# Kernel tuning notes

Hardware: AMD Instinct MI355X
Metric: run time of the kernel (lower is better)

Reference implementation:

```python
import jax, jax.numpy as jnp
import numpy as np

N = 50000; E = 200000; H = 128; L = 3; T = 2; FOUT = 64
G = 1000; NP = 3; ATOM_V = 64; BOND_V = 8
EPS = 1e-5
_DEG_HIST = np.array([0., 50000., 75000., 50000., 25000.])
# PyG PNAConv: avg_deg['log'] = sum(hist[d] * log(d+1)) / num_nodes
AVG_DEG_LOG = float((np.log(np.arange(5) + 1.0) * _DEG_HIST).sum() / _DEG_HIST.sum())


def _bn(v, g, b):
    # training-mode BatchNorm1d (biased variance), eps=1e-5
    mu = v.mean(0)
    var = ((v - mu) ** 2).mean(0)
    return (v - mu) * jax.lax.rsqrt(var + EPS) * g + b


def setup_inputs() -> dict:
    key = jax.random.key(0)
    ks = jax.random.split(key, 16)
    def nrm(k, shape, fan):
        return (jax.random.normal(k, shape, dtype=jnp.float32) / np.sqrt(fan)).astype(jnp.float32)
    return {
        'x': jax.random.randint(ks[0], (N, 9), 0, ATOM_V),
        'edge_index': jax.random.randint(ks[1], (2, E), 0, N),
        'batch': jnp.sort(jax.random.randint(ks[2], (N,), 0, G)),
        'edge_attr_idx': jax.random.randint(ks[3], (E, 3), 0, BOND_V),
        'atom_emb': nrm(ks[4], (9, ATOM_V, H), H),
        'bond_emb': nrm(ks[5], (3, BOND_V, H), H),
        'edge_W': nrm(ks[6], (L, H, H), H), 'edge_b': jnp.zeros((L, H), jnp.float32),
        'pre_W': nrm(ks[7], (L, T, 3 * H, H), 3 * H), 'pre_b': jnp.zeros((L, T, H), jnp.float32),
        'post_W': nrm(ks[8], (L, T, 13 * H, FOUT), 13 * H), 'post_b': jnp.zeros((L, T, FOUT), jnp.float32),
        'lin_W': nrm(ks[9], (L, H, H), H), 'lin_b': jnp.zeros((L, H), jnp.float32),
        'bn_g': jnp.ones((L, H), jnp.float32), 'bn_b': jnp.zeros((L, H), jnp.float32),
        'mlp_W': nrm(ks[10], (2, H, H), H), 'mlp_b': jnp.zeros((2, H), jnp.float32),
        'mlp_g': jnp.ones((2, H), jnp.float32), 'mlp_be': jnp.zeros((2, H), jnp.float32),
        'hW1': nrm(ks[11], (H, H // 2), H), 'hb1': jnp.zeros((H // 2,), jnp.float32),
        'hg1': jnp.ones((H // 2,), jnp.float32), 'hbe1': jnp.zeros((H // 2,), jnp.float32),
        'hW2': nrm(ks[12], (H // 2, H // 4), H // 2), 'hb2': jnp.zeros((H // 4,), jnp.float32),
        'hg2': jnp.ones((H // 4,), jnp.float32), 'hbe2': jnp.zeros((H // 4,), jnp.float32),
        'hW3': nrm(ks[13], (H // 4, NP), H // 4), 'hb3': jnp.zeros((NP,), jnp.float32),
    }


def reference(x, edge_index, batch, edge_attr_idx, atom_emb, bond_emb,
              edge_W, edge_b, pre_W, pre_b, post_W, post_b, lin_W, lin_b,
              bn_g, bn_b, mlp_W, mlp_b, mlp_g, mlp_be,
              hW1, hb1, hg1, hbe1, hW2, hb2, hg2, hbe2, hW3, hb3):
    # encoders: sum of per-feature embeddings (OGB Atom/Bond encoder)
    h = atom_emb[jnp.arange(9), x].sum(1)               # [N,H]
    e = bond_emb[jnp.arange(3), edge_attr_idx].sum(1)   # [E,H]
    src, dst = edge_index[0], edge_index[1]
    cnt = jax.ops.segment_sum(jnp.ones((E,), jnp.float32), dst, N)
    deg = jnp.maximum(cnt, 1.0)[:, None, None]          # clamp(1), as in PyG scalers
    amp = jnp.log(deg + 1.0) / AVG_DEG_LOG
    att = AVG_DEG_LOG / jnp.log(deg + 1.0)
    has = (cnt > 0)[:, None, None]
    for l in range(L):
        ea = e @ edge_W[l] + edge_b[l]                                  # [E,H]
        msg_in = jnp.concatenate([h[dst], h[src], ea], -1)              # [E,3H]
        m = jnp.einsum('ef,tfh->eth', msg_in, pre_W[l]) + pre_b[l]      # [E,T,H]
        s1 = jax.ops.segment_sum(m, dst, N)
        s2 = jax.ops.segment_sum(m * m, dst, N)
        mean = s1 / deg
        std = jnp.sqrt(jax.nn.relu(s2 / deg - mean * mean) + EPS)
        mn = jnp.where(has, jax.ops.segment_min(m, dst, N), 0.0)
        mx = jnp.where(has, jax.ops.segment_max(m, dst, N), 0.0)
        agg = jnp.concatenate([mean, mn, mx, std], -1)                  # [N,T,4H]
        scaled = jnp.concatenate([agg, agg * amp, agg * att], -1)       # [N,T,12H]
        upd = jnp.concatenate(
            [jnp.broadcast_to(h[:, None, :], (N, T, H)), scaled], -1)   # [N,T,13H]
        o = jnp.einsum('ntf,tfo->nto', upd, post_W[l]) + post_b[l]      # [N,T,FOUT]
        o = o.reshape(N, T * FOUT) @ lin_W[l] + lin_b[l]                # [N,H]
        h = jax.nn.relu(_bn(o, bn_g[l], bn_b[l]))
    g = jax.ops.segment_sum(h, batch, G)                                # [G,H]
    for i in range(2):
        g = jax.nn.relu(_bn(g @ mlp_W[i] + mlp_b[i], mlp_g[i], mlp_be[i]))
    g = jax.nn.relu(_bn(g @ hW1 + hb1, hg1, hbe1))
    g = jax.nn.relu(_bn(g @ hW2 + hb2, hg2, hbe2))
    return g @ hW3 + hb3                                                # [G,NP]
```

## Files before the change

### kernel.cpp

```cpp
#include <hip/hip_runtime.h>
#include <math.h>


#define NN 50000
#define NE 200000
#define HD 128
#define NG 1000
#define EPSV 1e-5f
#define ALOGC 1.1330197327247628f

#define AP 1288
#define OPF 132
#define SCB 49

typedef __bf16 bf16x8 __attribute__((ext_vector_type(8)));
typedef float f32x4 __attribute__((ext_vector_type(4)));

__device__ __forceinline__ unsigned short f2bf(float f) {
    unsigned int u = __float_as_uint(f);
    unsigned int r = (u + 0x7FFFu + ((u >> 16) & 1u)) >> 16;
    return (unsigned short)r;
}
__device__ __forceinline__ float bf2f(unsigned short h) {
    return __uint_as_float((unsigned int)h << 16);
}

__global__ void k_fill(float* __restrict__ o, float v, int n) {
    int i = blockIdx.x * 256 + threadIdx.x;
    if (i < n) o[i] = v;
}

__global__ void k_zero(float* __restrict__ z, int n) {
    int i = blockIdx.x * 256 + threadIdx.x;
    if (i < n) z[i] = 0.f;
}

__global__ __launch_bounds__(256) void k_encode_nodes(
    const int* __restrict__ x, const float* __restrict__ aemb, float* __restrict__ h) {
    __shared__ int xi[8][9];
    int nb = blockIdx.x * 8;
    int tid = threadIdx.x;
    if (tid < 72) xi[tid / 9][tid % 9] = x[nb * 9 + tid];
    __syncthreads();
    int node = tid >> 5, c4 = (tid & 31) * 4;
    float4 acc = make_float4(0.f, 0.f, 0.f, 0.f);
#pragma unroll
    for (int f = 0; f < 9; ++f) {
        float4 e = *(const float4*)(aemb + (size_t)(f * 64 + xi[node][f]) * HD + c4);
        acc.x += e.x; acc.y += e.y; acc.z += e.z; acc.w += e.w;
    }
    *(float4*)(h + (size_t)(nb + node) * HD + c4) = acc;
}

__global__ void k_count(const int* __restrict__ dst, int* __restrict__ cnt) {
    int e = blockIdx.x * 256 + threadIdx.x;
    if (e < NE) atomicAdd(&cnt[dst[e]], 1);
}

__global__ __launch_bounds__(1024) void k_scanA(const int* __restrict__ cnt,
                                                int* __restrict__ sc, int* __restrict__ tot) {
    __shared__ int buf[1024];
    int tid = threadIdx.x;
    int i = blockIdx.x * 1024 + tid;
    int v = (i < NN) ? cnt[i] : 0;
    buf[tid] = v;
    __syncthreads();
    for (int s = 1; s < 1024; s <<= 1) {
        int t = (tid >= s) ? buf[tid - s] : 0;
        __syncthreads();
        buf[tid] += t;
        __syncthreads();
    }
    if (i < NN) sc[i] = buf[tid];
    if (tid == 1023) tot[blockIdx.x] = buf[1023];
}

__global__ void k_scanB(const int* __restrict__ tot, int* __restrict__ offb) {
    if (threadIdx.x == 0) {
        int run = 0;
        for (int b = 0; b < SCB; ++b) { offb[b] = run; run += tot[b]; }
    }
}

__global__ __launch_bounds__(1024) void k_scanC(
    const int* __restrict__ cnt, const int* __restrict__ sc, const int* __restrict__ offb,
    int* __restrict__ rowptr, float* __restrict__ ampv, float* __restrict__ attv) {
    int i = blockIdx.x * 1024 + threadIdx.x;
    if (i == 0) rowptr[0] = 0;
    if (i < NN) {
        rowptr[i + 1] = offb[blockIdx.x] + sc[i];
        int v = cnt[i];
        float dg = (float)(v > 0 ? v : 1);
        float lg = logf(dg + 1.0f);
        ampv[i] = lg / ALOGC;
        attv[i] = ALOGC / lg;
    }
}

__global__ void k_scatter(const int* __restrict__ ei, const int* __restrict__ eai,
                          const int* __restrict__ rowptr,
                          int* __restrict__ fill, int* __restrict__ precs) {
    int e = blockIdx.x * 256 + threadIdx.x;
    if (e < NE) {
        int d = ei[NE + e];
        int pos = rowptr[d] + atomicAdd(&fill[d], 1);
        int cidx = eai[e * 3] | (eai[e * 3 + 1] << 3) | (eai[e * 3 + 2] << 6);
        precs[pos] = ei[e] | (cidx << 17);
    }
}

__global__ void k_fold(const float* __restrict__ edge_W, const float* __restrict__ edge_b,
                       const float* __restrict__ pre_W, const float* __restrict__ pre_b,
                       float* __restrict__ cW, float* __restrict__ tb) {
    int l = blockIdx.y;
    int k = blockIdx.x;
    int tj = threadIdx.x;
    int t = tj >> 7, j = tj & 127;
    const float* pw = pre_W + ((size_t)(l * 2 + t) * 384 + 256) * 128 + j;
    if (k < 128) {
        const float* ew = edge_W + ((size_t)l * 128 + k) * 128;
        float acc = 0.f;
        for (int i = 0; i < 128; ++i) acc += ew[i] * pw[i * 128];
        cW[((size_t)l * 128 + k) * 256 + tj] = acc;
    } else {
        const float* eb = edge_b + l * 128;
        float acc = pre_b[(l * 2 + t) * 128 + j];
        for (int i = 0; i < 128; ++i) acc += eb[i] * pw[i * 128];
        tb[l * 256 + tj] = acc;
    }
}

__global__ void k_bcomb2(const float* __restrict__ bemb, const float* __restrict__ cW,
                         unsigned short* __restrict__ bcomb) {
    int ci = blockIdx.x, l = blockIdx.y, tj = threadIdx.x;
    const float* s0 = bemb + (size_t)(0 * 8 + (ci & 7)) * 128;
    const float* s1 = bemb + (size_t)(1 * 8 + ((ci >> 3) & 7)) * 128;
    const float* s2 = bemb + (size_t)(2 * 8 + (ci >> 6)) * 128;
    const float* w = cW + (size_t)l * 128 * 256;
    float acc = 0.f;
    for (int i = 0; i < 128; ++i) acc += (s0[i] + s1[i] + s2[i]) * w[i * 256 + tj];
    bcomb[((size_t)l * 512 + ci) * 256 + tj] = f2bf(acc);
}

__device__ __forceinline__ void pack_body2(const float* __restrict__ W, int N, int NT,
                                           unsigned short* __restrict__ pkh,
                                           unsigned short* __restrict__ pkl,
                                           int blk, int lane) {
    int kstep = blk / NT, nt = blk - kstep * NT;
    int kb = kstep * 32 + (lane >> 4) * 8;
    int col = nt * 16 + (lane & 15);
    unsigned short th[8], tl[8];
#pragma unroll
    for (int i = 0; i < 8; ++i) {
        float w = W[(size_t)(kb + i) * N + col];
        unsigned short hh = f2bf(w);
        th[i] = hh;
        tl[i] = f2bf(w - bf2f(hh));
    }
    size_t base = ((size_t)blk * 64 + lane) * 8;
    *(uint4*)(pkh + base) = *(uint4*)th;
    *(uint4*)(pkl + base) = *(uint4*)tl;
}

__global__ __launch_bounds__(64) void k_packall(
    const float* __restrict__ post_W, const float* __restrict__ lin_W,
    const float* __restrict__ pre_W,
    unsigned short* __restrict__ pkPostHi, unsigned short* __restrict__ pkPostLo,
    unsigned short* __restrict__ pkLinHi, unsigned short* __restrict__ pkLinLo,
    unsigned short* __restrict__ pkPreHi, unsigned short* __restrict__ pkPreLo) {
    int b = blockIdx.x;
    int lane = threadIdx.x;
    if (b < 1248) {
        int l = b / 416, rem = b % 416;
        int t = rem / 208, blk = rem % 208;
        size_t off = ((size_t)l * 2 + t) * 106496;
        pack_body2(post_W + ((size_t)l * 2 + t) * 1664 * 64, 64, 4,
                   pkPostHi + off, pkPostLo + off, blk, lane);
    } else if (b < 1344) {
        int idx = b - 1248;
        int l = idx / 32, blk = idx % 32;
        pack_body2(lin_W + (size_t)l * 128 * 128, 128, 8,
                   pkLinHi + (size_t)l * 16384, pkLinLo + (size_t)l * 16384, blk, lane);
    } else {
        int idx = b - 1344;
        int l = idx / 128, bb = idx % 128;
        const float* preW = pre_W + (size_t)l * 2 * 384 * 128;
        unsigned short* phi = pkPreHi + (size_t)l * 65536;
        unsigned short* plo = pkPreLo + (size_t)l * 65536;
        int kstep = bb >> 5, nt = bb & 31;
        int q = lane >> 4, nc = lane & 15;
        int col = nt * 16 + nc;
        int t = (col >> 7) & 1;
        int jcol = col & 127;
        int fbase = (col < 256) ? 0 : 128;
        unsigned short hi[8], lo[8];
#pragma unroll
        for (int i = 0; i < 8; ++i) {
            int k = kstep * 32 + q * 8 + i;
            float w = preW[((size_t)t * 384 + fbase + k) * 128 + jcol];
            unsigned short h16 = f2bf(w);
            hi[i] = h16;
            lo[i] = f2bf(w - bf2f(h16));
        }
        size_t base = ((size_t)bb * 64 + lane) * 8;
        *(uint4*)(phi + base) = *(uint4*)hi;
        *(uint4*)(plo + base) = *(uint4*)lo;
    }
}

__device__ __forceinline__ void pre_mfma_body(
    const unsigned short* __restrict__ ah, const unsigned short* __restrict__ al,
    const unsigned short* __restrict__ phi, const unsigned short* __restrict__ plo,
    const float* __restrict__ tb, int n0, int tid,
    unsigned short* __restrict__ hzd, unsigned short* __restrict__ hzs) {
    int lane = tid & 63, w = tid >> 6;
    int q = lane >> 4, nc = lane & 15;
    f32x4 acc[8];
#pragma unroll
    for (int j = 0; j < 8; ++j) acc[j] = (f32x4){0.f, 0.f, 0.f, 0.f};
#pragma unroll
    for (int kk = 0; kk < 4; ++kk) {
        bf16x8 Ahi = *(const bf16x8*)(ah + nc * 136 + kk * 32 + q * 8);
        bf16x8 Alo = *(const bf16x8*)(al + nc * 136 + kk * 32 + q * 8);
#pragma unroll
        for (int j = 0; j < 8; ++j) {
            int nt = w * 8 + j;
            size_t base = ((size_t)(kk * 32 + nt) * 64 + lane) * 8;
            bf16x8 Bhi = *(const bf16x8*)(phi + base);
            bf16x8 Blo = *(const bf16x8*)(plo + base);
            acc[j] = __builtin_amdgcn_mfma_f32_16x16x32_bf16(Ahi, Bhi, acc[j], 0, 0, 0);
            acc[j] = __builtin_amdgcn_mfma_f32_16x16x32_bf16(Ahi, Blo, acc[j], 0, 0, 0);
            acc[j] = __builtin_amdgcn_mfma_f32_16x16x32_bf16(Alo, Bhi, acc[j], 0, 0, 0);
        }
    }
#pragma unroll
    for (int j = 0; j < 8; ++j) {
        int col = (w * 8 + j) * 16 + nc;
#pragma unroll
        for (int reg = 0; reg < 4; ++reg) {
            int row = n0 + q * 4 + reg;
            if (col < 256) hzd[(size_t)row * 256 + col] = f2bf(acc[j][reg] + tb[col]);
            else           hzs[(size_t)row * 256 + (col - 256)] = f2bf(acc[j][reg]);
        }
    }
}

__global__ __launch_bounds__(256) void k_pre_m(
    const float* __restrict__ h,
    const unsigned short* __restrict__ phi, const unsigned short* __restrict__ plo,
    const float* __restrict__ tb,
    unsigned short* __restrict__ hzd, unsigned short* __restrict__ hzs) {
    __shared__ __align__(16) unsigned short ah[16 * 136];
    __shared__ __align__(16) unsigned short al[16 * 136];
    int n0 = blockIdx.x * 16;
    int tid = threadIdx.x;
    {
        int node = tid >> 4, cg = (tid & 15) * 8;
        const float* hs = h + (size_t)(n0 + node) * HD + cg;
        float4 v0 = *(const float4*)(hs);
        float4 v1 = *(const float4*)(hs + 4);
        float vv[8] = {v0.x, v0.y, v0.z, v0.w, v1.x, v1.y, v1.z, v1.w};
        unsigned short hh[8], ll[8];
#pragma unroll
        for (int i = 0; i < 8; ++i) {
            hh[i] = f2bf(vv[i]);
            ll[i] = f2bf(vv[i] - bf2f(hh[i]));
        }
        *(uint4*)(ah + node * 136 + cg) = *(uint4*)hh;
        *(uint4*)(al + node * 136 + cg) = *(uint4*)ll;
    }
    __syncthreads();
    pre_mfma_body(ah, al, phi, plo, tb, n0, tid, hzd, hzs);
}

__global__ __launch_bounds__(256) void k_bnpre(
    const float* __restrict__ o2, const float* __restrict__ stats,
    const float* __restrict__ g, const float* __restrict__ b,
    const unsigned short* __restrict__ phi, const unsigned short* __restrict__ plo,
    const float* __restrict__ tb,
    float* __restrict__ h, unsigned short* __restrict__ hzd, unsigned short* __restrict__ hzs) {
    __shared__ __align__(16) unsigned short ah[16 * 136];
    __shared__ __align__(16) unsigned short al[16 * 136];
    int n0 = blockIdx.x * 16;
    int tid = threadIdx.x;
    {
        int node = tid >> 4, cg = (tid & 15) * 8;
        int n = n0 + node;
        const float* os = o2 + (size_t)n * HD + cg;
        float4 v0 = *(const float4*)(os);
        float4 v1 = *(const float4*)(os + 4);
        float vv[8] = {v0.x, v0.y, v0.z, v0.w, v1.x, v1.y, v1.z, v1.w};
        unsigned short hh[8], ll[8];
        float ou[8];
#pragma unroll
        for (int i = 0; i < 8; ++i) {
            int c = cg + i;
            float mu = stats[c] * (1.f / NN);
            float var = stats[128 + c] * (1.f / NN) - mu * mu;
            float val = (vv[i] - mu) * rsqrtf(var + EPSV) * g[c] + b[c];
            val = fmaxf(val, 0.f);
            ou[i] = val;
            hh[i] = f2bf(val);
            ll[i] = f2bf(val - bf2f(hh[i]));
        }
        float* hd = h + (size_t)n * HD + cg;
        *(float4*)(hd) = make_float4(ou[0], ou[1], ou[2], ou[3]);
        *(float4*)(hd + 4) = make_float4(ou[4], ou[5], ou[6], ou[7]);
        *(uint4*)(ah + node * 136 + cg) = *(uint4*)hh;
        *(uint4*)(al + node * 136 + cg) = *(uint4*)ll;
    }
    __syncthreads();
    pre_mfma_body(ah, al, phi, plo, tb, n0, tid, hzd, hzs);
}

__global__ __launch_bounds__(256) void k_post(
    const float* __restrict__ h,
    const unsigned short* __restrict__ hzd, const unsigned short* __restrict__ hzs,
    const int* __restrict__ rowptr, const int* __restrict__ precs,
    const unsigned short* __restrict__ bcomb,
    const float* __restrict__ ampv, const float* __restrict__ attv,
    const unsigned short* __restrict__ pkPostHi, const unsigned short* __restrict__ pkPostLo,
    const float* __restrict__ postb,
    const unsigned short* __restrict__ pkLinHi, const unsigned short* __restrict__ pkLinLo,
    const float* __restrict__ linb,
    float* __restrict__ o2, float* __restrict__ stats) {
    __shared__ __align__(16) unsigned short a_lds[16 * AP];
    __shared__ __align__(16) float o_f[16 * OPF];
    __shared__ float s_amp[16], s_att[16];
    int n0 = blockIdx.x * 16;
    int tid = threadIdx.x;

    {
        int node = tid >> 4, cg = (tid & 15) * 8;
        const float* hs = h + (size_t)(n0 + node) * HD + cg;
        float4 v0 = *(const float4*)(hs);
        float4 v1 = *(const float4*)(hs + 4);
        unsigned short* d0 = a_lds + node * AP + cg;
        unsigned short* d1 = d0 + 640;
        unsigned short bb[8];
        bb[0] = f2bf(v0.x); bb[1] = f2bf(v0.y); bb[2] = f2bf(v0.z); bb[3] = f2bf(v0.w);
        bb[4] = f2bf(v1.x); bb[5] = f2bf(v1.y); bb[6] = f2bf(v1.z); bb[7] = f2bf(v1.w);
#pragma unroll
        for (int i = 0; i < 8; ++i) { d0[i] = bb[i]; d1[i] = bb[i]; }
    }
    if (tid < 16) { s_amp[tid] = ampv[n0 + tid]; s_att[tid] = attv[n0 + tid]; }
    __syncthreads();

    {
        int wv = tid >> 6, lane = tid & 63;
        int cc = lane * 4;
        int tt = cc >> 7, jj = cc & 127;
        const float4 Z4 = make_float4(0.f, 0.f, 0.f, 0.f);
        const float4 BIG = make_float4(3.4e38f, 3.4e38f, 3.4e38f, 3.4e38f);
        const float4 NBIG = make_float4(-3.4e38f, -3.4e38f, -3.4e38f, -3.4e38f);

#define EDGE_ACC(P, S1, S2, MN, MX)                                                       \
        {                                                                                 \
            int rec = precs[(P)];                                                         \
            int sp = rec & 131071;                                                        \
            int ci = rec >> 17;                                                           \
            uint2 uv = *(const uint2*)(hzs + (size_t)sp * 256 + cc);                      \
            uint2 ub = *(const uint2*)(bcomb + (size_t)ci * 256 + cc);                    \
            float wx = __uint_as_float(uv.x << 16) + __uint_as_float(ub.x << 16);         \
            float wy = __uint_as_float(uv.x & 0xffff0000u) + __uint_as_float(ub.x & 0xffff0000u); \
            float wz = __uint_as_float(uv.y << 16) + __uint_as_float(ub.y << 16);         \
            float ww = __uint_as_float(uv.y & 0xffff0000u) + __uint_as_float(ub.y & 0xffff0000u); \
            S1.x += wx; S1.y += wy; S1.z += wz; S1.w += ww;                               \
            S2.x += wx * wx; S2.y += wy * wy; S2.z += wz * wz; S2.w += ww * ww;           \
            MN.x = fminf(MN.x, wx); MN.y = fminf(MN.y, wy);                               \
            MN.z = fminf(MN.z, wz); MN.w = fminf(MN.w, ww);                               \
            MX.x = fmaxf(MX.x, wx); MX.y = fmaxf(MX.y, wy);                               \
            MX.z = fmaxf(MX.z, wz); MX.w = fmaxf(MX.w, ww);                               \
        }

        auto fin = [&](int r, int cnt, float4 hd, float4 s1, float4 s2, float4 mn, float4 mx) {
            float inv = 1.f / (float)(cnt > 0 ? cnt : 1);
            float4 mw, stdv, mean;
            mw.x = s1.x * inv; mw.y = s1.y * inv; mw.z = s1.z * inv; mw.w = s1.w * inv;
            stdv.x = sqrtf(fmaxf(s2.x * inv - mw.x * mw.x, 0.f) + EPSV);
            stdv.y = sqrtf(fmaxf(s2.y * inv - mw.y * mw.y, 0.f) + EPSV);
            stdv.z = sqrtf(fmaxf(s2.z * inv - mw.z * mw.z, 0.f) + EPSV);
            stdv.w = sqrtf(fmaxf(s2.w * inv - mw.w * mw.w, 0.f) + EPSV);
            if (cnt > 0) {
                mean.x = hd.x + mw.x; mean.y = hd.y + mw.y;
                mean.z = hd.z + mw.z; mean.w = hd.w + mw.w;
                mn.x += hd.x; mn.y += hd.y; mn.z += hd.z; mn.w += hd.w;
                mx.x += hd.x; mx.y += hd.y; mx.z += hd.z; mx.w += hd.w;
            } else {
                mean = Z4; mn = Z4; mx = Z4;
            }
            unsigned short* d = a_lds + r * AP + tt * 640 + 128 + jj;
            d[0] = f2bf(mean.x); d[1] = f2bf(mean.y); d[2] = f2bf(mean.z); d[3] = f2bf(mean.w);
            d += 128; d[0] = f2bf(mn.x); d[1] = f2bf(mn.y); d[2] = f2bf(mn.z); d[3] = f2bf(mn.w);
            d += 128; d[0] = f2bf(mx.x); d[1] = f2bf(mx.y); d[2] = f2bf(mx.z); d[3] = f2bf(mx.w);
            d += 128; d[0] = f2bf(stdv.x); d[1] = f2bf(stdv.y); d[2] = f2bf(stdv.z); d[3] = f2bf(stdv.w);
        };

        for (int i = 0; i < 2; ++i) {
            int ra = wv * 4 + i * 2;
            int rb = ra + 1;
            int na = n0 + ra, nb = n0 + rb;
            int pa0 = rowptr[na], pa1 = rowptr[na + 1];
            int pb0 = rowptr[nb], pb1 = rowptr[nb + 1];
            uint2 uda = *(const uint2*)(hzd + (size_t)na * 256 + cc);
            uint2 udb = *(const uint2*)(hzd + (size_t)nb * 256 + cc);
            float4 hda, hdb;
            hda.x = __uint_as_float(uda.x << 16); hda.y = __uint_as_float(uda.x & 0xffff0000u);
            hda.z = __uint_as_float(uda.y << 16); hda.w = __uint_as_float(uda.y & 0xffff0000u);
            hdb.x = __uint_as_float(udb.x << 16); hdb.y = __uint_as_float(udb.x & 0xffff0000u);
            hdb.z = __uint_as_float(udb.y << 16); hdb.w = __uint_as_float(udb.y & 0xffff0000u);
            float4 s1a = Z4, s2a = Z4, mna = BIG, mxa = NBIG;
            float4 s1b = Z4, s2b = Z4, mnb = BIG, mxb = NBIG;
            int da = pa1 - pa0, db = pb1 - pb0;
            int mc = (da < db) ? da : db;
            for (int k = 0; k < mc; ++k) {
                EDGE_ACC(pa0 + k, s1a, s2a, mna, mxa)
                EDGE_ACC(pb0 + k, s1b, s2b, mnb, mxb)
            }
            for (int k = mc; k < da; ++k) EDGE_ACC(pa0 + k, s1a, s2a, mna, mxa)
            for (int k = mc; k < db; ++k) EDGE_ACC(pb0 + k, s1b, s2b, mnb, mxb)
            fin(ra, da, hda, s1a, s2a, mna, mxa);
            fin(rb, db, hdb, s1b, s2b, mnb, mxb);
        }
#undef EDGE_ACC
    }
    __syncthreads();

    {
        int lane = tid & 63;
        int w = tid >> 6;
        int t = w >> 1;
        int ntb = (w & 1) * 2;
        int q = lane >> 4, nc = lane & 15;
        const unsigned short* arow = a_lds + (size_t)nc * AP + t * 640 + q * 8;
        size_t toff = (size_t)t * 106496;
        const unsigned short* pkh = pkPostHi + toff;
        const unsigned short* pkl = pkPostLo + toff;
        f32x4 aP0 = {0.f, 0.f, 0.f, 0.f}, aP1 = {0.f, 0.f, 0.f, 0.f};
        f32x4 aA0 = {0.f, 0.f, 0.f, 0.f}, aA1 = {0.f, 0.f, 0.f, 0.f};
        f32x4 aT0 = {0.f, 0.f, 0.f, 0.f}, aT1 = {0.f, 0.f, 0.f, 0.f};
        for (int kk = 0; kk < 20; ++kk) {
            bf16x8 af = *(const bf16x8*)(arow + kk * 32);
            size_t ib = ((size_t)(kk * 4 + ntb) * 64 + lane) * 8;
            aP0 = __builtin_amdgcn_mfma_f32_16x16x32_bf16(af, *(const bf16x8*)(pkh + ib), aP0, 0, 0, 0);
            aP0 = __builtin_amdgcn_mfma_f32_16x16x32_bf16(af, *(const bf16x8*)(pkl + ib), aP0, 0, 0, 0);
            aP1 = __builtin_amdgcn_mfma_f32_16x16x32_bf16(af, *(const bf16x8*)(pkh + ib + 512), aP1, 0, 0, 0);
            aP1 = __builtin_amdgcn_mfma_f32_16x16x32_bf16(af, *(const bf16x8*)(pkl + ib + 512), aP1, 0, 0, 0);
            if (kk >= 4) {
                size_t ia = ((size_t)((kk + 16) * 4 + ntb) * 64 + lane) * 8;
                aA0 = __builtin_amdgcn_mfma_f32_16x16x32_bf16(af, *(const bf16x8*)(pkh + ia), aA0, 0, 0, 0);
                aA0 = __builtin_amdgcn_mfma_f32_16x16x32_bf16(af, *(const bf16x8*)(pkl + ia), aA0, 0, 0, 0);
                aA1 = __builtin_amdgcn_mfma_f32_16x16x32_bf16(af, *(const bf16x8*)(pkh + ia + 512), aA1, 0, 0, 0);
                aA1 = __builtin_amdgcn_mfma_f32_16x16x32_bf16(af, *(const bf16x8*)(pkl + ia + 512), aA1, 0, 0, 0);
                size_t it = ((size_t)((kk + 32) * 4 + ntb) * 64 + lane) * 8;
                aT0 = __builtin_amdgcn_mfma_f32_16x16x32_bf16(af, *(const bf16x8*)(pkh + it), aT0, 0, 0, 0);
                aT0 = __builtin_amdgcn_mfma_f32_16x16x32_bf16(af, *(const bf16x8*)(pkl + it), aT0, 0, 0, 0);
                aT1 = __builtin_amdgcn_mfma_f32_16x16x32_bf16(af, *(const bf16x8*)(pkh + it + 512), aT1, 0, 0, 0);
                aT1 = __builtin_amdgcn_mfma_f32_16x16x32_bf16(af, *(const bf16x8*)(pkl + it + 512), aT1, 0, 0, 0);
            }
        }
#pragma unroll
        for (int u = 0; u < 2; ++u) {
            int nt = ntb + u;
            int col = t * 64 + nt * 16 + nc;
            float pbia = postb[t * 64 + nt * 16 + nc];
            f32x4 P = u ? aP1 : aP0;
            f32x4 A = u ? aA1 : aA0;
            f32x4 T = u ? aT1 : aT0;
#pragma unroll
            for (int reg = 0; reg < 4; ++reg) {
                int mrow = q * 4 + reg;
                o_f[mrow * OPF + col] = P[reg] + s_amp[mrow] * A[reg] + s_att[mrow] * T[reg] + pbia;
            }
        }
    }
    __syncthreads();

    {
        int lane = tid & 63;
        int w = tid >> 6;
        int ntb = w * 2;
        int q = lane >> 4, nc = lane & 15;
        const float* arow = o_f + (size_t)nc * OPF + q * 8;
        f32x4 L0 = {0.f, 0.f, 0.f, 0.f}, L1 = {0.f, 0.f, 0.f, 0.f};
#pragma unroll
        for (int kk = 0; kk < 4; ++kk) {
            float4 a0 = *(const float4*)(arow + kk * 32);
            float4 a1 = *(const float4*)(arow + kk * 32 + 4);
            float vv[8] = {a0.x, a0.y, a0.z, a0.w, a1.x, a1.y, a1.z, a1.w};
            unsigned short hh[8], ll[8];
#pragma unroll
            for (int i = 0; i < 8; ++i) {
                hh[i] = f2bf(vv[i]);
                ll[i] = f2bf(vv[i] - bf2f(hh[i]));
            }
            bf16x8 Ahi = *(const bf16x8*)hh;
            bf16x8 Alo = *(const bf16x8*)ll;
            size_t ib = ((size_t)(kk * 8 + ntb) * 64 + lane) * 8;
            bf16x8 B0h = *(const bf16x8*)(pkLinHi + ib);
            bf16x8 B0l = *(const bf16x8*)(pkLinLo + ib);
            bf16x8 B1h = *(const bf16x8*)(pkLinHi + ib + 512);
            bf16x8 B1l = *(const bf16x8*)(pkLinLo + ib + 512);
            L0 = __builtin_amdgcn_mfma_f32_16x16x32_bf16(Ahi, B0h, L0, 0, 0, 0);
            L0 = __builtin_amdgcn_mfma_f32_16x16x32_bf16(Alo, B0h, L0, 0, 0, 0);
            L0 = __builtin_amdgcn_mfma_f32_16x16x32_bf16(Ahi, B0l, L0, 0, 0, 0);
            L1 = __builtin_amdgcn_mfma_f32_16x16x32_bf16(Ahi, B1h, L1, 0, 0, 0);
            L1 = __builtin_amdgcn_mfma_f32_16x16x32_bf16(Alo, B1h, L1, 0, 0, 0);
            L1 = __builtin_amdgcn_mfma_f32_16x16x32_bf16(Ahi, B1l, L1, 0, 0, 0);
        }
#pragma unroll
        for (int u = 0; u < 2; ++u) {
            int col = (ntb + u) * 16 + nc;
            float lb = linb[col];
            f32x4 L = u ? L1 : L0;
            float ps = 0.f, pss = 0.f;
#pragma unroll
            for (int reg = 0; reg < 4; ++reg) {
                int mrow = q * 4 + reg;
                float v = L[reg] + lb;
                o2[(size_t)(n0 + mrow) * HD + col] = v;
                ps += v; pss += v * v;
            }
            ps += __shfl_down(ps, 16); ps += __shfl_down(ps, 32);
            pss += __shfl_down(pss, 16); pss += __shfl_down(pss, 32);
            if (q == 0) {
                atomicAdd(&stats[col], ps);
                atomicAdd(&stats[128 + col], pss);
            }
        }
    }
}

__global__ void k_pool(const float* __restrict__ o2, const float* __restrict__ stats,
                       const float* __restrict__ g, const float* __restrict__ b,
                       const int* __restrict__ batch, float* __restrict__ g0) {
    int c = threadIdx.x;
    float mu = stats[c] * (1.f / NN);
    float var = stats[128 + c] * (1.f / NN) - mu * mu;
    float rs = rsqrtf(var + EPSV) * g[c];
    float bb = b[c];
    int nbase = blockIdx.x * 64;
    float run = 0.f; int cur = -1;
    for (int i = 0; i < 64; ++i) {
        int n = nbase + i;
        if (n >= NN) break;
        int bi = batch[n];
        if (bi != cur) {
            if (cur >= 0) atomicAdd(&g0[(size_t)cur * HD + c], run);
            cur = bi; run = 0.f;
        }
        run += fmaxf((o2[(size_t)n * HD + c] - mu) * rs + bb, 0.f);
    }
    if (cur >= 0) atomicAdd(&g0[(size_t)cur * HD + c], run);
}

__global__ void k_head_gemm(const float* __restrict__ x, const float* __restrict__ W,
                            const float* __restrict__ b, float* __restrict__ y,
                            float* __restrict__ stats, int K, int Kout) {
    int row = blockIdx.x;
    int col = threadIdx.x;
    if (col >= Kout) return;
    float acc = b[col];
    for (int k = 0; k < K; k += 4) {
        float4 xv = *(const float4*)(x + (size_t)row * K + k);
        acc += xv.x * W[(k + 0) * Kout + col] + xv.y * W[(k + 1) * Kout + col]
             + xv.z * W[(k + 2) * Kout + col] + xv.w * W[(k + 3) * Kout + col];
    }
    y[(size_t)row * Kout + col] = acc;
    if (stats) {
        atomicAdd(&stats[col], acc);
        atomicAdd(&stats[Kout + col], acc * acc);
    }
}

__global__ __launch_bounds__(128) void k_head_fused(
    const float* __restrict__ y_in, const float* __restrict__ stats_in,
    const float* __restrict__ g, const float* __restrict__ b,
    const float* __restrict__ W, const float* __restrict__ bias,
    float* __restrict__ y_out, float* __restrict__ stats_out, int Kin, int Kout) {
    __shared__ float row[128];
    int r = blockIdx.x, tid = threadIdx.x;
    if (tid < Kin) {
        float mu = stats_in[tid] * (1.f / NG);
        float var = stats_in[Kin + tid] * (1.f / NG) - mu * mu;
        float v = (y_in[(size_t)r * Kin + tid] - mu) * rsqrtf(var + EPSV) * g[tid] + b[tid];
        row[tid] = fmaxf(v, 0.f);
    }
    __syncthreads();
    if (tid < Kout) {
        float acc = bias[tid];
        for (int k = 0; k < Kin; ++k) acc += row[k] * W[(size_t)k * Kout + tid];
        y_out[(size_t)r * Kout + tid] = acc;
        if (stats_out) {
            atomicAdd(&stats_out[tid], acc);
            atomicAdd(&stats_out[Kout + tid], acc * acc);
        }
    }
}

extern "C" void kernel_launch(void* const* d_in, const int* in_sizes, int n_in,
                              void* d_out, int out_size, void* d_ws, size_t ws_size,
                              hipStream_t stream) {
    const int*   x        = (const int*)  d_in[0];
    const int*   ei       = (const int*)  d_in[1];
    const int*   batch    = (const int*)  d_in[2];
    const int*   eai      = (const int*)  d_in[3];
    const float* atom_emb = (const float*)d_in[4];
    const float* bond_emb = (const float*)d_in[5];
    const float* edge_W   = (const float*)d_in[6];
    const float* edge_b   = (const float*)d_in[7];
    const float* pre_W    = (const float*)d_in[8];
    const float* pre_b    = (const float*)d_in[9];
    const float* post_W   = (const float*)d_in[10];
    const float* post_b   = (const float*)d_in[11];
    const float* lin_W    = (const float*)d_in[12];
    const float* lin_b    = (const float*)d_in[13];
    const float* bn_g     = (const float*)d_in[14];
    const float* bn_b     = (const float*)d_in[15];
    const float* mlp_W    = (const float*)d_in[16];
    const float* mlp_b    = (const float*)d_in[17];
    const float* mlp_g    = (const float*)d_in[18];
    const float* mlp_be   = (const float*)d_in[19];
    const float* hW1 = (const float*)d_in[20]; const float* hb1  = (const float*)d_in[21];
    const float* hg1 = (const float*)d_in[22]; const float* hbe1 = (const float*)d_in[23];
    const float* hW2 = (const float*)d_in[24]; const float* hb2  = (const float*)d_in[25];
    const float* hg2 = (const float*)d_in[26]; const float* hbe2 = (const float*)d_in[27];
    const float* hW3 = (const float*)d_in[28]; const float* hb3  = (const float*)d_in[29];
    float* out = (float*)d_out;
    (void)n_in; (void)in_sizes;

    char* p = (char*)d_ws;
    size_t off = 0;
    auto alloc = [&](size_t bytes) -> char* {
        char* r = p + off;
        off += (bytes + 255) & ~(size_t)255;
        return r;
    };
    float* h     = (float*)alloc((size_t)NN * HD * 4);
    float* o2    = (float*)alloc((size_t)NN * HD * 4);
    unsigned short* hzd = (unsigned short*)alloc((size_t)NN * 256 * 2);
    unsigned short* hzs = (unsigned short*)alloc((size_t)NN * 256 * 2);
    float* ampv  = (float*)alloc((size_t)NN * 4);
    float* attv  = (float*)alloc((size_t)NN * 4);
    int*   rowptr= (int*)  alloc((size_t)(NN + 1) * 4);
    int*   precs = (int*)  alloc((size_t)NE * 4);
    int*   sc    = (int*)  alloc((size_t)NN * 4);
    int*   stot  = (int*)  alloc((size_t)SCB * 4);
    int*   soff  = (int*)  alloc((size_t)SCB * 4);
    float* cW    = (float*)alloc((size_t)3 * 128 * 256 * 4);
    float* tbb   = (float*)alloc((size_t)3 * 256 * 4);
    unsigned short* bcomb = (unsigned short*)alloc((size_t)3 * 512 * 256 * 2);
    unsigned short* pkPostHi = (unsigned short*)alloc((size_t)3 * 2 * 106496 * 2);
    unsigned short* pkPostLo = (unsigned short*)alloc((size_t)3 * 2 * 106496 * 2);
    unsigned short* pkLinHi  = (unsigned short*)alloc((size_t)3 * 16384 * 2);
    unsigned short* pkLinLo  = (unsigned short*)alloc((size_t)3 * 16384 * 2);
    unsigned short* pkPreHi  = (unsigned short*)alloc((size_t)3 * 65536 * 2);
    unsigned short* pkPreLo  = (unsigned short*)alloc((size_t)3 * 65536 * 2);
    float* gA    = (float*)alloc((size_t)NG * HD * 4);
    float* gB    = (float*)alloc((size_t)NG * HD * 4);
    char* z0 = p + off;
    int*   cnt   = (int*)  alloc((size_t)NN * 4);
    int*   fill  = (int*)  alloc((size_t)NN * 4);
    float* stats = (float*)alloc((size_t)3 * 256 * 4);
    float* hstats= (float*)alloc((size_t)4 * 256 * 4);
    float* g0    = (float*)alloc((size_t)NG * HD * 4);
    size_t zwords = (size_t)((p + off) - z0) / 4;

    if (off > ws_size) {
        k_fill<<<(out_size + 255) / 256, 256, 0, stream>>>(out, (float)ws_size, out_size);
        return;
    }

    k_zero<<<(int)((zwords + 255) / 256), 256, 0, stream>>>((float*)z0, (int)zwords);
    k_encode_nodes<<<NN / 8, 256, 0, stream>>>(x, atom_emb, h);
    k_count<<<(NE + 255) / 256, 256, 0, stream>>>(ei + NE, cnt);
    k_scanA<<<SCB, 1024, 0, stream>>>(cnt, sc, stot);
    k_scanB<<<1, 64, 0, stream>>>(stot, soff);
    k_scanC<<<SCB, 1024, 0, stream>>>(cnt, sc, soff, rowptr, ampv, attv);
    k_scatter<<<(NE + 255) / 256, 256, 0, stream>>>(ei, eai, rowptr, fill, precs);
    k_fold<<<dim3(129, 3), 256, 0, stream>>>(edge_W, edge_b, pre_W, pre_b, cW, tbb);
    k_bcomb2<<<dim3(512, 3), 256, 0, stream>>>(bond_emb, cW, bcomb);
    k_packall<<<1728, 64, 0, stream>>>(post_W, lin_W, pre_W,
        pkPostHi, pkPostLo, pkLinHi, pkLinLo, pkPreHi, pkPreLo);

    for (int l = 0; l < 3; ++l) {
        if (l == 0) {
            k_pre_m<<<NN / 16, 256, 0, stream>>>(h, pkPreHi, pkPreLo, tbb, hzd, hzs);
        } else {
            k_bnpre<<<NN / 16, 256, 0, stream>>>(o2, stats + (l - 1) * 256,
                bn_g + (l - 1) * 128, bn_b + (l - 1) * 128,
                pkPreHi + (size_t)l * 65536, pkPreLo + (size_t)l * 65536,
                tbb + l * 256, h, hzd, hzs);
        }
        k_post<<<NN / 16, 256, 0, stream>>>(h, hzd, hzs, rowptr, precs,
            bcomb + (size_t)l * 512 * 256,
            ampv, attv,
            pkPostHi + (size_t)l * 2 * 106496, pkPostLo + (size_t)l * 2 * 106496,
            post_b + l * 2 * 64,
            pkLinHi + (size_t)l * 16384, pkLinLo + (size_t)l * 16384,
            lin_b + l * 128,
            o2, stats + l * 256);
    }

    k_pool<<<(NN + 63) / 64, 128, 0, stream>>>(o2, stats + 2 * 256,
        bn_g + 2 * 128, bn_b + 2 * 128, batch, g0);

    k_head_gemm<<<NG, 128, 0, stream>>>(g0, mlp_W, mlp_b, gA, hstats, 128, 128);
    k_head_fused<<<NG, 128, 0, stream>>>(gA, hstats, mlp_g, mlp_be,
        mlp_W + 128 * 128, mlp_b + 128, gB, hstats + 256, 128, 128);
    k_head_fused<<<NG, 128, 0, stream>>>(gB, hstats + 256, mlp_g + 128, mlp_be + 128,
        hW1, hb1, gA, hstats + 512, 128, 64);
    k_head_fused<<<NG, 128, 0, stream>>>(gA, hstats + 512, hg1, hbe1,
        hW2, hb2, gB, hstats + 768, 64, 32);
    k_head_fused<<<NG, 128, 0, stream>>>(gB, hstats + 768, hg2, hbe2,
        hW3, hb3, out, (float*)nullptr, 32, 3);
}
```

Measured before the change: 946.7 us.

## Process 32 nodes per pre-GEMM block and stage edge records in LDS

The pre-transform MFMA kernels now handle 32 nodes per block with two accumulator sets, so each packed weight fragment loaded from global memory feeds twice as many MFMAs and the weight traffic per node is halved. Bounds checks cover the partial last block. Separately, the aggregation kernel preloads its block's edge records from precs into shared memory (up to 512) and falls back to global reads when a block has more edges than that. The costs are higher register pressure from the doubled accumulators, half as many blocks for the pre kernels, and an extra LDS fill step before aggregation.

```diff
diff --git a/kernel.cpp b/kernel.cpp
--- a/kernel.cpp
+++ b/kernel.cpp
@@ -11,6 +11,7 @@
 
 #define AP 1288
 #define OPF 132
+#define ECAP 512
 #define SCB 49
 
 typedef __bf16 bf16x8 __attribute__((ext_vector_type(8)));
@@ -208,39 +209,54 @@
     }
 }
 
-__device__ __forceinline__ void pre_mfma_body(
+__device__ __forceinline__ void pre_mfma_body2(
     const unsigned short* __restrict__ ah, const unsigned short* __restrict__ al,
     const unsigned short* __restrict__ phi, const unsigned short* __restrict__ plo,
     const float* __restrict__ tb, int n0, int tid,
     unsigned short* __restrict__ hzd, unsigned short* __restrict__ hzs) {
     int lane = tid & 63, w = tid >> 6;
     int q = lane >> 4, nc = lane & 15;
-    f32x4 acc[8];
-#pragma unroll
-    for (int j = 0; j < 8; ++j) acc[j] = (f32x4){0.f, 0.f, 0.f, 0.f};
+    f32x4 acc0[8], acc1[8];
+#pragma unroll
+    for (int j = 0; j < 8; ++j) {
+        acc0[j] = (f32x4){0.f, 0.f, 0.f, 0.f};
+        acc1[j] = (f32x4){0.f, 0.f, 0.f, 0.f};
+    }
 #pragma unroll
     for (int kk = 0; kk < 4; ++kk) {
-        bf16x8 Ahi = *(const bf16x8*)(ah + nc * 136 + kk * 32 + q * 8);
-        bf16x8 Alo = *(const bf16x8*)(al + nc * 136 + kk * 32 + q * 8);
+        bf16x8 Ahi0 = *(const bf16x8*)(ah + nc * 136 + kk * 32 + q * 8);
+        bf16x8 Alo0 = *(const bf16x8*)(al + nc * 136 + kk * 32 + q * 8);
+        bf16x8 Ahi1 = *(const bf16x8*)(ah + (16 + nc) * 136 + kk * 32 + q * 8);
+        bf16x8 Alo1 = *(const bf16x8*)(al + (16 + nc) * 136 + kk * 32 + q * 8);
 #pragma unroll
         for (int j = 0; j < 8; ++j) {
             int nt = w * 8 + j;
             size_t base = ((size_t)(kk * 32 + nt) * 64 + lane) * 8;
             bf16x8 Bhi = *(const bf16x8*)(phi + base);
             bf16x8 Blo = *(const bf16x8*)(plo + base);
-            acc[j] = __builtin_amdgcn_mfma_f32_16x16x32_bf16(Ahi, Bhi, acc[j], 0, 0, 0);
-            acc[j] = __builtin_amdgcn_mfma_f32_16x16x32_bf16(Ahi, Blo, acc[j], 0, 0, 0);
-            acc[j] = __builtin_amdgcn_mfma_f32_16x16x32_bf16(Alo, Bhi, acc[j], 0, 0, 0);
+            acc0[j] = __builtin_amdgcn_mfma_f32_16x16x32_bf16(Ahi0, Bhi, acc0[j], 0, 0, 0);
+            acc0[j] = __builtin_amdgcn_mfma_f32_16x16x32_bf16(Ahi0, Blo, acc0[j], 0, 0, 0);
+            acc0[j] = __builtin_amdgcn_mfma_f32_16x16x32_bf16(Alo0, Bhi, acc0[j], 0, 0, 0);
+            acc1[j] = __builtin_amdgcn_mfma_f32_16x16x32_bf16(Ahi1, Bhi, acc1[j], 0, 0, 0);
+            acc1[j] = __builtin_amdgcn_mfma_f32_16x16x32_bf16(Ahi1, Blo, acc1[j], 0, 0, 0);
+            acc1[j] = __builtin_amdgcn_mfma_f32_16x16x32_bf16(Alo1, Bhi, acc1[j], 0, 0, 0);
         }
     }
 #pragma unroll
     for (int j = 0; j < 8; ++j) {
         int col = (w * 8 + j) * 16 + nc;
+        float bias = (col < 256) ? tb[col] : 0.f;
 #pragma unroll
         for (int reg = 0; reg < 4; ++reg) {
-            int row = n0 + q * 4 + reg;
-            if (col < 256) hzd[(size_t)row * 256 + col] = f2bf(acc[j][reg] + tb[col]);
-            else           hzs[(size_t)row * 256 + (col - 256)] = f2bf(acc[j][reg]);
+            int r0 = n0 + q * 4 + reg;
+            int r1 = r0 + 16;
+            if (col < 256) {
+                if (r0 < NN) hzd[(size_t)r0 * 256 + col] = f2bf(acc0[j][reg] + bias);
+                if (r1 < NN) hzd[(size_t)r1 * 256 + col] = f2bf(acc1[j][reg] + bias);
+            } else {
+                if (r0 < NN) hzs[(size_t)r0 * 256 + (col - 256)] = f2bf(acc0[j][reg]);
+                if (r1 < NN) hzs[(size_t)r1 * 256 + (col - 256)] = f2bf(acc1[j][reg]);
+            }
         }
     }
 }
@@ -250,27 +266,31 @@
     const unsigned short* __restrict__ phi, const unsigned short* __restrict__ plo,
     const float* __restrict__ tb,
     unsigned short* __restrict__ hzd, unsigned short* __restrict__ hzs) {
-    __shared__ __align__(16) unsigned short ah[16 * 136];
-    __shared__ __align__(16) unsigned short al[16 * 136];
-    int n0 = blockIdx.x * 16;
+    __shared__ __align__(16) unsigned short ah[32 * 136];
+    __shared__ __align__(16) unsigned short al[32 * 136];
+    int n0 = blockIdx.x * 32;
     int tid = threadIdx.x;
-    {
-        int node = tid >> 4, cg = (tid & 15) * 8;
-        const float* hs = h + (size_t)(n0 + node) * HD + cg;
-        float4 v0 = *(const float4*)(hs);
-        float4 v1 = *(const float4*)(hs + 4);
-        float vv[8] = {v0.x, v0.y, v0.z, v0.w, v1.x, v1.y, v1.z, v1.w};
-        unsigned short hh[8], ll[8];
-#pragma unroll
-        for (int i = 0; i < 8; ++i) {
-            hh[i] = f2bf(vv[i]);
-            ll[i] = f2bf(vv[i] - bf2f(hh[i]));
+    for (int half = 0; half < 2; ++half) {
+        int node = (tid >> 4) + half * 16, cg = (tid & 15) * 8;
+        int n = n0 + node;
+        unsigned short hh[8] = {0, 0, 0, 0, 0, 0, 0, 0};
+        unsigned short ll[8] = {0, 0, 0, 0, 0, 0, 0, 0};
+        if (n < NN) {
+            const float* hs = h + (size_t)n * HD + cg;
+            float4 v0 = *(const float4*)(hs);
+            float4 v1 = *(const float4*)(hs + 4);
+            float vv[8] = {v0.x, v0.y, v0.z, v0.w, v1.x, v1.y, v1.z, v1.w};
+#pragma unroll
+            for (int i = 0; i < 8; ++i) {
+                hh[i] = f2bf(vv[i]);
+                ll[i] = f2bf(vv[i] - bf2f(hh[i]));
+            }
         }
         *(uint4*)(ah + node * 136 + cg) = *(uint4*)hh;
         *(uint4*)(al + node * 136 + cg) = *(uint4*)ll;
     }
     __syncthreads();
-    pre_mfma_body(ah, al, phi, plo, tb, n0, tid, hzd, hzs);
+    pre_mfma_body2(ah, al, phi, plo, tb, n0, tid, hzd, hzs);
 }
 
 __global__ __launch_bounds__(256) void k_bnpre(
@@ -279,38 +299,41 @@
     const unsigned short* __restrict__ phi, const unsigned short* __restrict__ plo,
     const float* __restrict__ tb,
     float* __restrict__ h, unsigned short* __restrict__ hzd, unsigned short* __restrict__ hzs) {
-    __shared__ __align__(16) unsigned short ah[16 * 136];
-    __shared__ __align__(16) unsigned short al[16 * 136];
-    int n0 = blockIdx.x * 16;
+    __shared__ __align__(16) unsigned short ah[32 * 136];
+    __shared__ __align__(16) unsigned short al[32 * 136];
+    int n0 = blockIdx.x * 32;
     int tid = threadIdx.x;
-    {
-        int node = tid >> 4, cg = (tid & 15) * 8;
+    for (int half = 0; half < 2; ++half) {
+        int node = (tid >> 4) + half * 16, cg = (tid & 15) * 8;
         int n = n0 + node;
-        const float* os = o2 + (size_t)n * HD + cg;
-        float4 v0 = *(const float4*)(os);
-        float4 v1 = *(const float4*)(os + 4);
-        float vv[8] = {v0.x, v0.y, v0.z, v0.w, v1.x, v1.y, v1.z, v1.w};
-        unsigned short hh[8], ll[8];
-        float ou[8];
-#pragma unroll
-        for (int i = 0; i < 8; ++i) {
-            int c = cg + i;
-            float mu = stats[c] * (1.f / NN);
-            float var = stats[128 + c] * (1.f / NN) - mu * mu;
-            float val = (vv[i] - mu) * rsqrtf(var + EPSV) * g[c] + b[c];
-            val = fmaxf(val, 0.f);
-            ou[i] = val;
-            hh[i] = f2bf(val);
-            ll[i] = f2bf(val - bf2f(hh[i]));
-        }
-        float* hd = h + (size_t)n * HD + cg;
-        *(float4*)(hd) = make_float4(ou[0], ou[1], ou[2], ou[3]);
-        *(float4*)(hd + 4) = make_float4(ou[4], ou[5], ou[6], ou[7]);
+        unsigned short hh[8] = {0, 0, 0, 0, 0, 0, 0, 0};
+        unsigned short ll[8] = {0, 0, 0, 0, 0, 0, 0, 0};
+        if (n < NN) {
+            const float* os = o2 + (size_t)n * HD + cg;
+            float4 v0 = *(const float4*)(os);
+            float4 v1 = *(const float4*)(os + 4);
+            float vv[8] = {v0.x, v0.y, v0.z, v0.w, v1.x, v1.y, v1.z, v1.w};
+            float ou[8];
+#pragma unroll
+            for (int i = 0; i < 8; ++i) {
+                int c = cg + i;
+                float mu = stats[c] * (1.f / NN);
+                float var = stats[128 + c] * (1.f / NN) - mu * mu;
+                float val = (vv[i] - mu) * rsqrtf(var + EPSV) * g[c] + b[c];
+                val = fmaxf(val, 0.f);
+                ou[i] = val;
+                hh[i] = f2bf(val);
+                ll[i] = f2bf(val - bf2f(hh[i]));
+            }
+            float* hd = h + (size_t)n * HD + cg;
+            *(float4*)(hd) = make_float4(ou[0], ou[1], ou[2], ou[3]);
+            *(float4*)(hd + 4) = make_float4(ou[4], ou[5], ou[6], ou[7]);
+        }
         *(uint4*)(ah + node * 136 + cg) = *(uint4*)hh;
         *(uint4*)(al + node * 136 + cg) = *(uint4*)ll;
     }
     __syncthreads();
-    pre_mfma_body(ah, al, phi, plo, tb, n0, tid, hzd, hzs);
+    pre_mfma_body2(ah, al, phi, plo, tb, n0, tid, hzd, hzs);
 }
 
 __global__ __launch_bounds__(256) void k_post(
@@ -326,10 +349,14 @@
     float* __restrict__ o2, float* __restrict__ stats) {
     __shared__ __align__(16) unsigned short a_lds[16 * AP];
     __shared__ __align__(16) float o_f[16 * OPF];
+    __shared__ int es[ECAP];
     __shared__ float s_amp[16], s_att[16];
     int n0 = blockIdx.x * 16;
     int tid = threadIdx.x;
 
+    int pbase = rowptr[n0];
+    int ecount = rowptr[n0 + 16] - pbase;
+    for (int i = tid; i < ecount && i < ECAP; i += 256) es[i] = precs[pbase + i];
     {
         int node = tid >> 4, cg = (tid & 15) * 8;
         const float* hs = h + (size_t)(n0 + node) * HD + cg;
@@ -350,13 +377,14 @@
         int wv = tid >> 6, lane = tid & 63;
         int cc = lane * 4;
         int tt = cc >> 7, jj = cc & 127;
+        bool incap = (ecount <= ECAP);
         const float4 Z4 = make_float4(0.f, 0.f, 0.f, 0.f);
         const float4 BIG = make_float4(3.4e38f, 3.4e38f, 3.4e38f, 3.4e38f);
         const float4 NBIG = make_float4(-3.4e38f, -3.4e38f, -3.4e38f, -3.4e38f);
 
 #define EDGE_ACC(P, S1, S2, MN, MX)                                                       \
         {                                                                                 \
-            int rec = precs[(P)];                                                         \
+            int rec = incap ? es[(P) - pbase] : precs[(P)];                               \
             int sp = rec & 131071;                                                        \
             int ci = rec >> 17;                                                           \
             uint2 uv = *(const uint2*)(hzs + (size_t)sp * 256 + cc);                      \
@@ -683,11 +711,12 @@
     k_packall<<<1728, 64, 0, stream>>>(post_W, lin_W, pre_W,
         pkPostHi, pkPostLo, pkLinHi, pkLinLo, pkPreHi, pkPreLo);
 
+    int preBlocks = (NN + 31) / 32;
     for (int l = 0; l < 3; ++l) {
         if (l == 0) {
-            k_pre_m<<<NN / 16, 256, 0, stream>>>(h, pkPreHi, pkPreLo, tbb, hzd, hzs);
+            k_pre_m<<<preBlocks, 256, 0, stream>>>(h, pkPreHi, pkPreLo, tbb, hzd, hzs);
         } else {
-            k_bnpre<<<NN / 16, 256, 0, stream>>>(o2, stats + (l - 1) * 256,
+            k_bnpre<<<preBlocks, 256, 0, stream>>>(o2, stats + (l - 1) * 256,
                 bn_g + (l - 1) * 128, bn_b + (l - 1) * 128,
                 pkPreHi + (size_t)l * 65536, pkPreLo + (size_t)l * 65536,
                 tbb + l * 256, h, hzd, hzs);
```

Measured after the change: 924.9 us (median of 2 runs). 1.02x faster.
